# Performance work log

Hardware: AMD Instinct MI355X
Metric: run time of the kernel (lower is better)

## Reference

```python
import jax, jax.numpy as jnp
import numpy as np

DIM = 1024
HEADS = 16
DIM_HEAD = 64
INNER = HEADS * DIM_HEAD  # 1024
SCALE = DIM_HEAD ** -0.5


def layernorm(x, gamma, beta, eps=1e-5):
    mu = jnp.mean(x, axis=-1, keepdims=True)
    var = jnp.var(x, axis=-1, keepdims=True)
    return (x - mu) * jax.lax.rsqrt(var + eps) * gamma + beta


def setup_inputs() -> dict:
    key = jax.random.key(0)
    ks = jax.random.split(key, 6)
    x = jax.random.normal(ks[0], (2, 2048, DIM), dtype=jnp.float32)
    # params (stored [in, out]; torch Linear does x @ W.T with W [out, in])
    w_q = jax.random.normal(ks[1], (DIM, INNER), dtype=jnp.float32) * (DIM ** -0.5)
    w_kv = jax.random.normal(ks[2], (DIM, 2 * INNER), dtype=jnp.float32) * (DIM ** -0.5)
    w_out = jax.random.normal(ks[3], (INNER, DIM), dtype=jnp.float32) * (INNER ** -0.5)
    b_out = jnp.zeros((DIM,), dtype=jnp.float32)
    gamma = jnp.ones((DIM,), dtype=jnp.float32)
    beta = jnp.zeros((DIM,), dtype=jnp.float32)
    return {"x": x, "w_q": w_q, "w_kv": w_kv, "w_out": w_out, "b_out": b_out,
            "gamma": gamma, "beta": beta}


def reference(x, w_q, w_kv, w_out, b_out, gamma, beta):
    b, n, _ = x.shape
    xn = layernorm(x, gamma, beta)
    q = xn @ w_q                           # [b, n, inner]
    kv = xn @ w_kv                         # [b, n, 2*inner]
    k, v = jnp.split(kv, 2, axis=-1)
    def split_heads(t):
        return t.reshape(b, n, HEADS, DIM_HEAD).transpose(0, 2, 1, 3)  # b h n d
    q, k, v = split_heads(q), split_heads(k), split_heads(v)
    dots = jnp.einsum('bhid,bhjd->bhij', q, k) * SCALE   # [b, h, n, n]
    attn = jax.nn.softmax(dots, axis=-1)
    out = jnp.einsum('bhij,bhjd->bhid', attn, v)          # [b, h, n, d]
    out = out.transpose(0, 2, 1, 3).reshape(b, n, INNER)  # b n (h d)
    return out @ w_out + b_out
```

## Files before the change

### kernel.cpp

```cpp
#include <hip/hip_runtime.h>

typedef unsigned short u16;
typedef u16   u16x8 __attribute__((ext_vector_type(8)));
typedef __bf16 bf16x8 __attribute__((ext_vector_type(8)));
typedef float f32x4 __attribute__((ext_vector_type(4)));
typedef float f32x2 __attribute__((ext_vector_type(2)));
typedef _Float16 f16x4 __attribute__((ext_vector_type(4)));
typedef _Float16 f16x8 __attribute__((ext_vector_type(8)));
typedef unsigned u32x2 __attribute__((ext_vector_type(2)));
typedef unsigned u32x4 __attribute__((ext_vector_type(4)));

__device__ __forceinline__ u16 f2b(float f){ __bf16 h=(__bf16)f; return __builtin_bit_cast(u16,h); }

__device__ __forceinline__ float ex2(float x){
#if __has_builtin(__builtin_amdgcn_exp2f)
  return __builtin_amdgcn_exp2f(x);
#else
  float r; asm("v_exp_f32 %0, %1" : "=v"(r) : "v"(x)); return r;
#endif
}

__device__ __forceinline__ f32x4 mfma16(u16x8 a, u16x8 b, f32x4 c){
  return __builtin_amdgcn_mfma_f32_16x16x32_bf16(
      __builtin_bit_cast(bf16x8,a), __builtin_bit_cast(bf16x8,b), c, 0,0,0);
}

__device__ __forceinline__ f32x4 mfma32h(f16x8 a, f16x8 b, f32x4 c){
  return __builtin_amdgcn_mfma_f32_16x16x32_f16(a, b, c, 0,0,0);
}

__device__ __forceinline__ void gl2lds16(const u16* g, u16* l){
  __builtin_amdgcn_global_load_lds((const __attribute__((address_space(1))) void*)g,
                                   (__attribute__((address_space(3))) void*)l, 16, 0, 0);
}

__global__ __launch_bounds__(256) void ln_kernel(const float* __restrict__ x,
                                                 const float* __restrict__ gamma,
                                                 const float* __restrict__ beta,
                                                 u16* __restrict__ xn){
  const int row = blockIdx.x, t = threadIdx.x;
  const float4 v = ((const float4*)(x + (size_t)row*1024))[t];
  float s  = v.x+v.y+v.z+v.w;
  float sq = v.x*v.x+v.y*v.y+v.z*v.z+v.w*v.w;
  for (int m=1;m<64;m<<=1){ s += __shfl_xor(s,m); sq += __shfl_xor(sq,m); }
  __shared__ float red[8];
  const int w=t>>6, l=t&63;
  if(l==0){ red[w]=s; red[4+w]=sq; }
  __syncthreads();
  const float S  = red[0]+red[1]+red[2]+red[3];
  const float SQ = red[4]+red[5]+red[6]+red[7];
  const float mu = S*(1.f/1024.f);
  const float var= SQ*(1.f/1024.f)-mu*mu;
  const float rs = rsqrtf(var+1e-5f);
  const float4 g4=((const float4*)gamma)[t], b4=((const float4*)beta)[t];
  u16 o0=f2b((v.x-mu)*rs*g4.x+b4.x);
  u16 o1=f2b((v.y-mu)*rs*g4.y+b4.y);
  u16 o2=f2b((v.z-mu)*rs*g4.z+b4.z);
  u16 o3=f2b((v.w-mu)*rs*g4.w+b4.w);
  uint2 p; p.x=(unsigned)o0|((unsigned)o1<<16); p.y=(unsigned)o2|((unsigned)o3<<16);
  ((uint2*)(xn + (size_t)row*1024))[t]=p;
}

__global__ __launch_bounds__(256) void wtrans_all_kernel(const float* __restrict__ wq,
    const float* __restrict__ wkv, const float* __restrict__ wout,
    u16* __restrict__ wqkvt, u16* __restrict__ woutt){
  __shared__ float tile[64][65];
  const int bx=blockIdx.x, t=threadIdx.x;
  const float* in; u16* out; int C, cxx;
  if(bx<16){ in=wq;  out=wqkvt;           C=1024; cxx=bx; }
  else if(bx<48){ in=wkv; out=wqkvt+1024*1024; C=2048; cxx=bx-16; }
  else { in=wout; out=woutt;             C=1024; cxx=bx-48; }
  const int R=1024;
  const int c0=cxx*64, r0=blockIdx.y*64;
  {
    const int r=t>>2, cc=t&3;
    const float* gp = in + (size_t)(r0+r)*C + c0 + cc*16;
    #pragma unroll
    for(int i=0;i<4;i++){
      float4 f=((const float4*)gp)[i];
      tile[r][cc*16+i*4+0]=f.x; tile[r][cc*16+i*4+1]=f.y;
      tile[r][cc*16+i*4+2]=f.z; tile[r][cc*16+i*4+3]=f.w;
    }
  }
  __syncthreads();
  const int c=t>>2, rc=t&3;
  u16x8 a,b;
  #pragma unroll
  for(int i=0;i<8;i++) a[i]=f2b(tile[rc*16+i][c]);
  #pragma unroll
  for(int i=0;i<8;i++) b[i]=f2b(tile[rc*16+8+i][c]);
  u16* op = out + (size_t)(c0+c)*R + r0 + rc*16;
  *(u16x8*)op=a; *(u16x8*)(op+8)=b;
}

template<int MODE,int TM>
__global__ __launch_bounds__(256) void gemm_bt_kernel(const u16* __restrict__ A,
    const u16* __restrict__ Bt, u16* __restrict__ outQ, u16* __restrict__ outK,
    u16* __restrict__ outV, float* __restrict__ outF, const float* __restrict__ bias,
    float scale, int M, int N, int K){
  constexpr int MT = TM/32;
  __shared__ u16 As[TM*64];
  __shared__ u16 Bs[128*64];
  const int t=threadIdx.x, w=t>>6, l=t&63, qd=l>>4, ln=l&15;
  const int m0=blockIdx.y*TM, n0=blockIdx.x*128;
  const int wm=(w>>1)*(TM/2), wn=(w&1)*64;
  f32x4 acc[MT][4] = {};
  const int nK = K>>6;
  for(int kt=0; kt<nK; kt++){
    const int k0=kt*64;
    #pragma unroll
    for(int p=0;p<MT;p++){
      const int cid=p*256+t, r=cid>>3, pc=cid&7, g=pc^(r&7);
      gl2lds16(A + (size_t)(m0+r)*K + k0 + g*8, &As[(p*256 + (t&192))*8]);
    }
    #pragma unroll
    for(int p=0;p<4;p++){
      const int cid=p*256+t, r=cid>>3, pc=cid&7, g=pc^(r&7);
      gl2lds16(Bt + (size_t)(n0+r)*K + k0 + g*8, &Bs[(p*256 + (t&192))*8]);
    }
    __syncthreads();
    #pragma unroll
    for(int ks=0;ks<2;ks++){
      u16x8 af[MT], bf[4];
      #pragma unroll
      for(int mt=0;mt<MT;mt++){
        const int m=wm+mt*16+ln, kc=ks*4+qd, pcc=kc^(m&7);
        af[mt]=*(const u16x8*)&As[m*64 + pcc*8];
      }
      #pragma unroll
      for(int nt=0;nt<4;nt++){
        const int n=wn+nt*16+ln, kc=ks*4+qd, pcc=kc^(n&7);
        bf[nt]=*(const u16x8*)&Bs[n*64 + pcc*8];
      }
      #pragma unroll
      for(int mt=0;mt<MT;mt++)
        #pragma unroll
        for(int nt=0;nt<4;nt++)
          acc[mt][nt]=mfma16(af[mt],bf[nt],acc[mt][nt]);
    }
    __syncthreads();
  }
  if(MODE==1){
    #pragma unroll
    for(int mt=0;mt<MT;mt++)
      #pragma unroll
      for(int rr=0;rr<4;rr++){
        const int row = m0+wm+mt*16+qd*4+rr;
        #pragma unroll
        for(int nt=0;nt<4;nt++){
          const int col = n0+wn+nt*16+ln;
          outF[(size_t)row*N+col]=acc[mt][nt][rr]+bias[col];
        }
      }
  } else if(n0<1024){
    #pragma unroll
    for(int mt=0;mt<MT;mt++)
      #pragma unroll
      for(int rr=0;rr<4;rr++){
        const int row = m0+wm+mt*16+qd*4+rr;
        #pragma unroll
        for(int nt=0;nt<4;nt++)
          outQ[(size_t)row*1024 + n0+wn+nt*16+ln]=f2b(acc[mt][nt][rr]*scale);
      }
  } else if(n0<2048){
    u16* kp = outK + (size_t)((m0>>11)*16 + ((n0-1024+wn)>>6))*131072;
    const int jb = (m0&2047) + wm;
    #pragma unroll
    for(int mt=0;mt<MT;mt++)
      #pragma unroll
      for(int rr=0;rr<4;rr++){
        const int j = jb + mt*16 + qd*4 + rr;
        #pragma unroll
        for(int nt=0;nt<4;nt++)
          kp[(size_t)j*64 + nt*16+ln]=f2b(acc[mt][nt][rr]);
      }
  } else {
    u16* vpp = outV + (size_t)((m0>>11)*16 + ((n0-2048+wn)>>6))*131072;
    const int jb = (m0&2047) + wm;
    #pragma unroll
    for(int mt=0;mt<MT;mt++){
      const int j = jb + mt*16 + qd*4;
      const int grp = (j>>5)*4 + ((j>>3)&3);
      const int sub = j&7;
      #pragma unroll
      for(int nt=0;nt<4;nt++){
        const auto lo=__builtin_amdgcn_cvt_pkrtz(acc[mt][nt][0],acc[mt][nt][1]);
        const auto hi=__builtin_amdgcn_cvt_pkrtz(acc[mt][nt][2],acc[mt][nt][3]);
        uint2 w2; w2.x=__builtin_bit_cast(unsigned,lo); w2.y=__builtin_bit_cast(unsigned,hi);
        *(uint2*)&vpp[(size_t)(grp*64 + nt*16+ln)*8 + sub] = w2;
      }
    }
  }
}

__global__ __launch_bounds__(512,4) void attn_kernel(const u16* __restrict__ Q,
    const u16* __restrict__ Kp, const u16* __restrict__ Vp, u16* __restrict__ O){
  __shared__ u16 Ks[2][8192];
  __shared__ u16 Vs[2][8192];
  const int qt=blockIdx.x, h=blockIdx.y, bb=blockIdx.z;
  const int t=threadIdx.x, w=t>>6, l=t&63, qd=l>>4, ln=l&15;
  const int q0=qt*128;
  const size_t baseQ=(size_t)bb*2048*1024 + h*64;
  const size_t baseKV=(size_t)(bb*16+h)*131072;
  u16x8 qf[2];
  #pragma unroll
  for(int ks=0;ks<2;ks++)
    qf[ks] = *(const u16x8*)(Q + baseQ + (size_t)(q0+w*16+ln)*1024 + ks*32+qd*8);
  f32x4 o_acc[4]={};
  f32x4 l_acc={};
  const f16x8 onesB={(_Float16)1.f,(_Float16)1.f,(_Float16)1.f,(_Float16)1.f,
                     (_Float16)1.f,(_Float16)1.f,(_Float16)1.f,(_Float16)1.f};
  const f32x4 zf={0.f,0.f,0.f,0.f};

  int koff[2];
  #pragma unroll
  for(int p=0;p<2;p++){
    const int r=(p*512+t)>>3, g=(t&7)^(r&7);
    const int pr=(r&~31)+((r>>2)&3)*8+((r>>4)&1)*4+(r&3);
    koff[p]=pr*64+g*8;
  }

  auto stage=[&](int buf,int j0){
    #pragma unroll
    for(int p=0;p<2;p++)
      gl2lds16(Kp + baseKV + (size_t)j0*64 + koff[p], &Ks[buf][(p*512+(t&448))*8]);
    #pragma unroll
    for(int p=0;p<2;p++)
      gl2lds16(Vp + baseKV + (size_t)(j0>>5)*2048 + (size_t)(p*512+t)*8,
               &Vs[buf][(p*512+(t&448))*8]);
  };

  stage(0,0);
  __syncthreads();
  int cur=0;
  for(int jt=0;jt<16;jt++){
    if(jt<15) stage(cur^1,(jt+1)*128);
    const u16* Kb=&Ks[cur][0];
    const u16* Vb=&Vs[cur][0];
    #pragma unroll
    for(int jh=0;jh<2;jh++){
      f16x8 vall[2][4];
      #pragma unroll
      for(int al=0;al<2;al++)
        #pragma unroll
        for(int dt=0;dt<4;dt++)
          vall[al][dt]=*(const f16x8*)&Vb[(((jh*2+al)*4+qd)*64 + dt*16+ln)*8];
      f32x4 s[4];
      #pragma unroll
      for(int ks=0;ks<2;ks++){
        u16x8 kf[4];
        #pragma unroll
        for(int j4=0;j4<4;j4++){
          const int row=(jh*4+j4)*16+ln;
          kf[j4]=*(const u16x8*)&Kb[row*64 + (((ks*4+qd)^(ln&7))*8)];
        }
        __builtin_amdgcn_s_setprio(1);
        #pragma unroll
        for(int j4=0;j4<4;j4++)
          s[j4] = ks? mfma16(kf[j4],qf[1],s[j4]) : mfma16(kf[j4],qf[0],zf);
        __builtin_amdgcn_s_setprio(0);
      }
      #pragma unroll
      for(int al=0;al<2;al++){
        const int t0=al*2, t1=al*2+1;
        u32x4 pw;
        pw.x=__builtin_bit_cast(unsigned,__builtin_amdgcn_cvt_pkrtz(ex2(s[t0][0]),ex2(s[t0][1])));
        pw.y=__builtin_bit_cast(unsigned,__builtin_amdgcn_cvt_pkrtz(ex2(s[t0][2]),ex2(s[t0][3])));
        pw.z=__builtin_bit_cast(unsigned,__builtin_amdgcn_cvt_pkrtz(ex2(s[t1][0]),ex2(s[t1][1])));
        pw.w=__builtin_bit_cast(unsigned,__builtin_amdgcn_cvt_pkrtz(ex2(s[t1][2]),ex2(s[t1][3])));
        const f16x8 pf=__builtin_bit_cast(f16x8,pw);
        __builtin_amdgcn_s_setprio(1);
        l_acc=mfma32h(pf,onesB,l_acc);
        #pragma unroll
        for(int dt=0;dt<4;dt++)
          o_acc[dt]=mfma32h(pf,vall[al][dt],o_acc[dt]);
        __builtin_amdgcn_s_setprio(0);
      }
    }
    __syncthreads();
    cur^=1;
  }

  #pragma unroll
  for(int rr=0;rr<4;rr++){
    const float lr=1.f/l_acc[rr];
    const int row=q0+w*16+qd*4+rr;
    #pragma unroll
    for(int dt=0;dt<4;dt++)
      O[baseQ + (size_t)row*1024 + dt*16+ln]=f2b(o_acc[dt][rr]*lr);
  }
}

extern "C" void kernel_launch(void* const* d_in, const int* in_sizes, int n_in,
                              void* d_out, int out_size, void* d_ws, size_t ws_size,
                              hipStream_t stream) {
  const float* x     = (const float*)d_in[0];
  const float* w_q   = (const float*)d_in[1];
  const float* w_kv  = (const float*)d_in[2];
  const float* w_out = (const float*)d_in[3];
  const float* b_out = (const float*)d_in[4];
  const float* gamma = (const float*)d_in[5];
  const float* beta  = (const float*)d_in[6];
  float* out = (float*)d_out;

  char* ws=(char*)d_ws;
  size_t off=0;
  u16* xn    =(u16*)(ws+off); off += (size_t)4096*1024*2;
  u16* wqkvt =(u16*)(ws+off); off += (size_t)3072*1024*2;
  u16* woutt =(u16*)(ws+off); off += (size_t)1024*1024*2;
  u16* qb    =(u16*)(ws+off); off += (size_t)4096*1024*2;
  u16* kpb   =(u16*)(ws+off); off += (size_t)4096*1024*2;
  u16* vpb   =(u16*)(ws+off); off += (size_t)4096*1024*2;
  u16* ob    =(u16*)(ws+off); off += (size_t)4096*1024*2;

  ln_kernel<<<4096,256,0,stream>>>(x,gamma,beta,xn);
  wtrans_all_kernel<<<dim3(64,16),256,0,stream>>>(w_q,w_kv,w_out,wqkvt,woutt);

  const float SCALE_Q = 0.125f*1.4426950408889634f;
  gemm_bt_kernel<2,128><<<dim3(24,32),256,0,stream>>>(xn,wqkvt,qb,kpb,vpb,nullptr,nullptr,SCALE_Q,4096,3072,1024);
  attn_kernel<<<dim3(16,16,2),512,0,stream>>>(qb,kpb,vpb,ob);
  gemm_bt_kernel<1,128><<<dim3(8,32),256,0,stream>>>(ob,woutt,nullptr,nullptr,nullptr,out,b_out,1.f,4096,1024,1024);
}
```

Baseline: 195.9 us.

## Merge prep kernels, double attention query rows per wave, shrink out-proj tile

Merges the layernorm and weight-transpose launches into one prep kernel that dispatches on block index, saving a launch. The attention kernel now gives each wave 32 query rows in two 16-row sub-tiles, so every K and V fragment read from LDS feeds twice as many MFMAs. This halves the attention grid to 256 blocks and raises register pressure. The output projection switches to a 64-row tile with twice as many blocks to improve occupancy.

```diff
diff --git a/kernel.cpp b/kernel.cpp
--- a/kernel.cpp
+++ b/kernel.cpp
@@ -34,44 +34,44 @@
                                    (__attribute__((address_space(3))) void*)l, 16, 0, 0);
 }
 
-__global__ __launch_bounds__(256) void ln_kernel(const float* __restrict__ x,
-                                                 const float* __restrict__ gamma,
-                                                 const float* __restrict__ beta,
-                                                 u16* __restrict__ xn){
-  const int row = blockIdx.x, t = threadIdx.x;
-  const float4 v = ((const float4*)(x + (size_t)row*1024))[t];
-  float s  = v.x+v.y+v.z+v.w;
-  float sq = v.x*v.x+v.y*v.y+v.z*v.z+v.w*v.w;
-  for (int m=1;m<64;m<<=1){ s += __shfl_xor(s,m); sq += __shfl_xor(sq,m); }
-  __shared__ float red[8];
-  const int w=t>>6, l=t&63;
-  if(l==0){ red[w]=s; red[4+w]=sq; }
-  __syncthreads();
-  const float S  = red[0]+red[1]+red[2]+red[3];
-  const float SQ = red[4]+red[5]+red[6]+red[7];
-  const float mu = S*(1.f/1024.f);
-  const float var= SQ*(1.f/1024.f)-mu*mu;
-  const float rs = rsqrtf(var+1e-5f);
-  const float4 g4=((const float4*)gamma)[t], b4=((const float4*)beta)[t];
-  u16 o0=f2b((v.x-mu)*rs*g4.x+b4.x);
-  u16 o1=f2b((v.y-mu)*rs*g4.y+b4.y);
-  u16 o2=f2b((v.z-mu)*rs*g4.z+b4.z);
-  u16 o3=f2b((v.w-mu)*rs*g4.w+b4.w);
-  uint2 p; p.x=(unsigned)o0|((unsigned)o1<<16); p.y=(unsigned)o2|((unsigned)o3<<16);
-  ((uint2*)(xn + (size_t)row*1024))[t]=p;
-}
-
-__global__ __launch_bounds__(256) void wtrans_all_kernel(const float* __restrict__ wq,
-    const float* __restrict__ wkv, const float* __restrict__ wout,
+__global__ __launch_bounds__(256) void prep_kernel(const float* __restrict__ x,
+    const float* __restrict__ gamma, const float* __restrict__ beta, u16* __restrict__ xn,
+    const float* __restrict__ wq, const float* __restrict__ wkv, const float* __restrict__ wout,
     u16* __restrict__ wqkvt, u16* __restrict__ woutt){
   __shared__ float tile[64][65];
-  const int bx=blockIdx.x, t=threadIdx.x;
+  __shared__ float red[8];
+  const int bid=blockIdx.x, t=threadIdx.x;
+  if(bid<4096){
+    const int row=bid;
+    const float4 v = ((const float4*)(x + (size_t)row*1024))[t];
+    float s  = v.x+v.y+v.z+v.w;
+    float sq = v.x*v.x+v.y*v.y+v.z*v.z+v.w*v.w;
+    for (int m=1;m<64;m<<=1){ s += __shfl_xor(s,m); sq += __shfl_xor(sq,m); }
+    const int w=t>>6, l=t&63;
+    if(l==0){ red[w]=s; red[4+w]=sq; }
+    __syncthreads();
+    const float S  = red[0]+red[1]+red[2]+red[3];
+    const float SQ = red[4]+red[5]+red[6]+red[7];
+    const float mu = S*(1.f/1024.f);
+    const float var= SQ*(1.f/1024.f)-mu*mu;
+    const float rs = rsqrtf(var+1e-5f);
+    const float4 g4=((const float4*)gamma)[t], b4=((const float4*)beta)[t];
+    u16 o0=f2b((v.x-mu)*rs*g4.x+b4.x);
+    u16 o1=f2b((v.y-mu)*rs*g4.y+b4.y);
+    u16 o2=f2b((v.z-mu)*rs*g4.z+b4.z);
+    u16 o3=f2b((v.w-mu)*rs*g4.w+b4.w);
+    uint2 p; p.x=(unsigned)o0|((unsigned)o1<<16); p.y=(unsigned)o2|((unsigned)o3<<16);
+    ((uint2*)(xn + (size_t)row*1024))[t]=p;
+    return;
+  }
+  const int wb=bid-4096;
+  const int bx=wb&63, by=wb>>6;
   const float* in; u16* out; int C, cxx;
   if(bx<16){ in=wq;  out=wqkvt;           C=1024; cxx=bx; }
   else if(bx<48){ in=wkv; out=wqkvt+1024*1024; C=2048; cxx=bx-16; }
   else { in=wout; out=woutt;             C=1024; cxx=bx-48; }
   const int R=1024;
-  const int c0=cxx*64, r0=blockIdx.y*64;
+  const int c0=cxx*64, r0=by*64;
   {
     const int r=t>>2, cc=t&3;
     const float* gp = in + (size_t)(r0+r)*C + c0 + cc*16;
@@ -199,15 +199,17 @@
   __shared__ u16 Vs[2][8192];
   const int qt=blockIdx.x, h=blockIdx.y, bb=blockIdx.z;
   const int t=threadIdx.x, w=t>>6, l=t&63, qd=l>>4, ln=l&15;
-  const int q0=qt*128;
+  const int q0=qt*256;
   const size_t baseQ=(size_t)bb*2048*1024 + h*64;
   const size_t baseKV=(size_t)(bb*16+h)*131072;
-  u16x8 qf[2];
-  #pragma unroll
-  for(int ks=0;ks<2;ks++)
-    qf[ks] = *(const u16x8*)(Q + baseQ + (size_t)(q0+w*16+ln)*1024 + ks*32+qd*8);
-  f32x4 o_acc[4]={};
-  f32x4 l_acc={};
+  u16x8 qf[2][2];
+  #pragma unroll
+  for(int sub=0;sub<2;sub++)
+    #pragma unroll
+    for(int ks=0;ks<2;ks++)
+      qf[sub][ks] = *(const u16x8*)(Q + baseQ + (size_t)(q0+w*32+sub*16+ln)*1024 + ks*32+qd*8);
+  f32x4 o_acc[2][4]={};
+  f32x4 l_acc[2]={};
   const f16x8 onesB={(_Float16)1.f,(_Float16)1.f,(_Float16)1.f,(_Float16)1.f,
                      (_Float16)1.f,(_Float16)1.f,(_Float16)1.f,(_Float16)1.f};
   const f32x4 zf={0.f,0.f,0.f,0.f};
@@ -239,42 +241,44 @@
     const u16* Vb=&Vs[cur][0];
     #pragma unroll
     for(int jh=0;jh<2;jh++){
-      f16x8 vall[2][4];
-      #pragma unroll
-      for(int al=0;al<2;al++)
-        #pragma unroll
-        for(int dt=0;dt<4;dt++)
-          vall[al][dt]=*(const f16x8*)&Vb[(((jh*2+al)*4+qd)*64 + dt*16+ln)*8];
-      f32x4 s[4];
+      f32x4 s[2][4];
       #pragma unroll
       for(int ks=0;ks<2;ks++){
         u16x8 kf[4];
         #pragma unroll
+        for(int j4=0;j4<4;j4++)
+          kf[j4]=*(const u16x8*)&Kb[((jh*4+j4)*16+ln)*64 + (((ks*4+qd)^(ln&7))*8)];
+        __builtin_amdgcn_s_setprio(1);
+        #pragma unroll
         for(int j4=0;j4<4;j4++){
-          const int row=(jh*4+j4)*16+ln;
-          kf[j4]=*(const u16x8*)&Kb[row*64 + (((ks*4+qd)^(ln&7))*8)];
+          s[0][j4] = ks? mfma16(kf[j4],qf[0][1],s[0][j4]) : mfma16(kf[j4],qf[0][0],zf);
+          s[1][j4] = ks? mfma16(kf[j4],qf[1][1],s[1][j4]) : mfma16(kf[j4],qf[1][0],zf);
         }
-        __builtin_amdgcn_s_setprio(1);
-        #pragma unroll
-        for(int j4=0;j4<4;j4++)
-          s[j4] = ks? mfma16(kf[j4],qf[1],s[j4]) : mfma16(kf[j4],qf[0],zf);
         __builtin_amdgcn_s_setprio(0);
       }
       #pragma unroll
       for(int al=0;al<2;al++){
-        const int t0=al*2, t1=al*2+1;
-        u32x4 pw;
-        pw.x=__builtin_bit_cast(unsigned,__builtin_amdgcn_cvt_pkrtz(ex2(s[t0][0]),ex2(s[t0][1])));
-        pw.y=__builtin_bit_cast(unsigned,__builtin_amdgcn_cvt_pkrtz(ex2(s[t0][2]),ex2(s[t0][3])));
-        pw.z=__builtin_bit_cast(unsigned,__builtin_amdgcn_cvt_pkrtz(ex2(s[t1][0]),ex2(s[t1][1])));
-        pw.w=__builtin_bit_cast(unsigned,__builtin_amdgcn_cvt_pkrtz(ex2(s[t1][2]),ex2(s[t1][3])));
-        const f16x8 pf=__builtin_bit_cast(f16x8,pw);
-        __builtin_amdgcn_s_setprio(1);
-        l_acc=mfma32h(pf,onesB,l_acc);
+        const int a=jh*2+al;
+        f16x8 vv[4];
         #pragma unroll
         for(int dt=0;dt<4;dt++)
-          o_acc[dt]=mfma32h(pf,vall[al][dt],o_acc[dt]);
-        __builtin_amdgcn_s_setprio(0);
+          vv[dt]=*(const f16x8*)&Vb[((a*4+qd)*64 + dt*16+ln)*8];
+        #pragma unroll
+        for(int sub=0;sub<2;sub++){
+          const int t0=al*2, t1=al*2+1;
+          u32x4 pw;
+          pw.x=__builtin_bit_cast(unsigned,__builtin_amdgcn_cvt_pkrtz(ex2(s[sub][t0][0]),ex2(s[sub][t0][1])));
+          pw.y=__builtin_bit_cast(unsigned,__builtin_amdgcn_cvt_pkrtz(ex2(s[sub][t0][2]),ex2(s[sub][t0][3])));
+          pw.z=__builtin_bit_cast(unsigned,__builtin_amdgcn_cvt_pkrtz(ex2(s[sub][t1][0]),ex2(s[sub][t1][1])));
+          pw.w=__builtin_bit_cast(unsigned,__builtin_amdgcn_cvt_pkrtz(ex2(s[sub][t1][2]),ex2(s[sub][t1][3])));
+          const f16x8 pf=__builtin_bit_cast(f16x8,pw);
+          __builtin_amdgcn_s_setprio(1);
+          l_acc[sub]=mfma32h(pf,onesB,l_acc[sub]);
+          #pragma unroll
+          for(int dt=0;dt<4;dt++)
+            o_acc[sub][dt]=mfma32h(pf,vv[dt],o_acc[sub][dt]);
+          __builtin_amdgcn_s_setprio(0);
+        }
       }
     }
     __syncthreads();
@@ -282,13 +286,15 @@
   }
 
   #pragma unroll
-  for(int rr=0;rr<4;rr++){
-    const float lr=1.f/l_acc[rr];
-    const int row=q0+w*16+qd*4+rr;
-    #pragma unroll
-    for(int dt=0;dt<4;dt++)
-      O[baseQ + (size_t)row*1024 + dt*16+ln]=f2b(o_acc[dt][rr]*lr);
-  }
+  for(int sub=0;sub<2;sub++)
+    #pragma unroll
+    for(int rr=0;rr<4;rr++){
+      const float lr=1.f/l_acc[sub][rr];
+      const int row=q0+w*32+sub*16+qd*4+rr;
+      #pragma unroll
+      for(int dt=0;dt<4;dt++)
+        O[baseQ + (size_t)row*1024 + dt*16+ln]=f2b(o_acc[sub][dt][rr]*lr);
+    }
 }
 
 extern "C" void kernel_launch(void* const* d_in, const int* in_sizes, int n_in,
@@ -313,11 +319,10 @@
   u16* vpb   =(u16*)(ws+off); off += (size_t)4096*1024*2;
   u16* ob    =(u16*)(ws+off); off += (size_t)4096*1024*2;
 
-  ln_kernel<<<4096,256,0,stream>>>(x,gamma,beta,xn);
-  wtrans_all_kernel<<<dim3(64,16),256,0,stream>>>(w_q,w_kv,w_out,wqkvt,woutt);
+  prep_kernel<<<5120,256,0,stream>>>(x,gamma,beta,xn,w_q,w_kv,w_out,wqkvt,woutt);
 
   const float SCALE_Q = 0.125f*1.4426950408889634f;
   gemm_bt_kernel<2,128><<<dim3(24,32),256,0,stream>>>(xn,wqkvt,qb,kpb,vpb,nullptr,nullptr,SCALE_Q,4096,3072,1024);
-  attn_kernel<<<dim3(16,16,2),512,0,stream>>>(qb,kpb,vpb,ob);
-  gemm_bt_kernel<1,128><<<dim3(8,32),256,0,stream>>>(ob,woutt,nullptr,nullptr,nullptr,out,b_out,1.f,4096,1024,1024);
-}
+  attn_kernel<<<dim3(8,16,2),512,0,stream>>>(qb,kpb,vpb,ob);
+  gemm_bt_kernel<1,64><<<dim3(8,64),256,0,stream>>>(ob,woutt,nullptr,nullptr,nullptr,out,b_out,1.f,4096,1024,1024);
+}
```

Result: faster. 178.8 us (-8.8%).
